# Performance work log

Hardware: AMD Instinct MI355X
Metric: run time of the kernel (lower is better)

Reference implementation:

```python
import jax, jax.numpy as jnp
import numpy as np

N, D, HF, HS, E, TOPK = 4096, 1024, 2048, 4096, 8, 2
NUM_FRACTAL = 4  # int(8 * 0.5)
EPS_RMS = 1e-6


def setup_inputs() -> dict:
    key = jax.random.key(0)
    ks = jax.random.split(key, 9)
    s = 0.02
    return {
        "x": jax.random.normal(ks[0], (N, D), dtype=jnp.float32),
        "router_w": jax.random.normal(ks[1], (E, D), dtype=jnp.float32) * s,
        "frac_rms": jnp.ones((NUM_FRACTAL, D), jnp.float32),
        "frac_w1": jax.random.normal(ks[2], (NUM_FRACTAL, HF, D), dtype=jnp.float32) * s,
        "frac_w2": jax.random.normal(ks[3], (NUM_FRACTAL, D, HF), dtype=jnp.float32) * s,
        "frac_w3": jax.random.normal(ks[4], (NUM_FRACTAL, HF, D), dtype=jnp.float32) * s,
        "frac_gamma": jnp.full((NUM_FRACTAL, D), 1e-5, jnp.float32),
        "sw_w1": jax.random.normal(ks[5], (E - NUM_FRACTAL, HS, D), dtype=jnp.float32) * s,
        "sw_w2": jax.random.normal(ks[6], (E - NUM_FRACTAL, D, HS), dtype=jnp.float32) * s,
        "sw_w3": jax.random.normal(ks[7], (E - NUM_FRACTAL, HS, D), dtype=jnp.float32) * s,
    }


def _rmsnorm(x, w):
    return x * jax.lax.rsqrt(jnp.mean(x * x, axis=-1, keepdims=True) + EPS_RMS) * w


def _swiglu(x, w1, w2, w3):
    # torch Linear: y = x @ W.T
    return (jax.nn.silu(x @ w1.T) * (x @ w3.T)) @ w2.T


def _fractal(x, rms_w, w1, w2, w3, gamma):
    # depth=1 FractalBlock, eval mode (stochastic depth = identity)
    xn = _rmsnorm(x, rms_w)
    xn = xn + _swiglu(xn, w1, w2, w3)
    return gamma * xn + x


def _moe(x, router_w, frac_rms, frac_w1, frac_w2, frac_w3, frac_gamma,
         sw_w1, sw_w2, sw_w3):
    gate_logits = x @ router_w.T                      # [N, E]
    weights = jax.nn.softmax(gate_logits, axis=-1)
    top_w, top_i = jax.lax.top_k(weights, TOPK)        # [N, K]
    top_w = top_w / jnp.maximum(jnp.sum(top_w, axis=-1, keepdims=True), 1e-9)
    # dense combine weights: zero for unrouted experts (mathematically equal
    # to the gather/index_add dispatch in the original)
    combine = jnp.zeros((x.shape[0], E), x.dtype).at[
        jnp.arange(x.shape[0])[:, None], top_i].add(top_w)  # [N, E]

    out = jnp.zeros_like(x)
    for e in range(NUM_FRACTAL):
        out = out + combine[:, e:e + 1] * _fractal(
            x, frac_rms[e], frac_w1[e], frac_w2[e], frac_w3[e], frac_gamma[e])
    for j in range(E - NUM_FRACTAL):
        e = NUM_FRACTAL + j
        out = out + combine[:, e:e + 1] * _swiglu(x, sw_w1[j], sw_w2[j], sw_w3[j])
    return out


def reference(x, router_w, frac_rms, frac_w1, frac_w2, frac_w3, frac_gamma,
              sw_w1, sw_w2, sw_w3):
    return _moe(x, router_w, frac_rms, frac_w1, frac_w2, frac_w3, frac_gamma,
                sw_w1, sw_w2, sw_w3)
```

## Files before the change

### kernel.cpp

```cpp
#include <hip/hip_runtime.h>
#include <stdint.h>

#define N_TOK 4096
#define DIM   1024
#define HFRAC 2048
#define HSW   4096
#define NEXP  8
#define NFRAC 4
#define TOPK  2
#define TOTAL_ROWS (N_TOK * TOPK)
#define PAD_ROWS   (TOTAL_ROWS + 128)

typedef unsigned short u16;
typedef __bf16 bf16x8 __attribute__((ext_vector_type(8)));
typedef float  floatx4 __attribute__((ext_vector_type(4)));

struct alignas(8)  us4 { u16 v[4]; };

__device__ __forceinline__ u16 f32_to_bf16_raw(float f) {
    union { float f; uint32_t u; } v; v.f = f;
    uint32_t u = v.u;
    uint32_t r = 0x7FFFu + ((u >> 16) & 1u);
    return (u16)((u + r) >> 16);
}
__device__ __forceinline__ float bf16_raw_to_f32(u16 h) {
    union { uint32_t u; float f; } v; v.u = ((uint32_t)h) << 16;
    return v.f;
}

__device__ __forceinline__ void gload16(const void* g, void* l) {
    __builtin_amdgcn_global_load_lds(
        (const __attribute__((address_space(1))) void*)g,
        (__attribute__((address_space(3))) void*)l, 16, 0, 0);
}

__device__ __forceinline__ int sw_addr(int row, int chunk) {
    return row * 64 + ((chunk ^ (row & 7)) << 3);
}

__global__ __launch_bounds__(256) void router_kernel(
    const float* __restrict__ x, const float* __restrict__ rw,
    int* __restrict__ re, float* __restrict__ rc, int* __restrict__ counts) {
    const int token = blockIdx.x * 4 + (threadIdx.x >> 6);
    const int lane  = threadIdx.x & 63;
    const float* xr = x + (size_t)token * DIM;

    float acc[NEXP];
#pragma unroll
    for (int e = 0; e < NEXP; ++e) acc[e] = 0.0f;
#pragma unroll
    for (int i = 0; i < DIM / 64; ++i) {
        int k = lane + i * 64;
        float xv = xr[k];
#pragma unroll
        for (int e = 0; e < NEXP; ++e) acc[e] += xv * rw[e * DIM + k];
    }
#pragma unroll
    for (int e = 0; e < NEXP; ++e) {
#pragma unroll
        for (int off = 32; off > 0; off >>= 1) acc[e] += __shfl_down(acc[e], off);
    }
    if (lane == 0) {
        float mx = acc[0];
#pragma unroll
        for (int e = 1; e < NEXP; ++e) mx = fmaxf(mx, acc[e]);
        float w[NEXP]; float s = 0.0f;
#pragma unroll
        for (int e = 0; e < NEXP; ++e) { w[e] = expf(acc[e] - mx); s += w[e]; }
        float inv = 1.0f / s;
#pragma unroll
        for (int e = 0; e < NEXP; ++e) w[e] *= inv;
        int i1 = 0;
#pragma unroll
        for (int e = 1; e < NEXP; ++e) if (w[e] > w[i1]) i1 = e;
        int i2 = (i1 == 0) ? 1 : 0;
#pragma unroll
        for (int e = 0; e < NEXP; ++e) if (e != i1 && w[e] > w[i2]) i2 = e;
        float denom = fmaxf(w[i1] + w[i2], 1e-9f);
        re[token]         = i1; rc[token]         = w[i1] / denom;
        re[N_TOK + token] = i2; rc[N_TOK + token] = w[i2] / denom;
        atomicAdd(&counts[i1], 1);
        atomicAdd(&counts[i2], 1);
    }
}

__global__ void offsets_kernel(const int* __restrict__ counts,
                               int* __restrict__ offs) {
    if (threadIdx.x == 0 && blockIdx.x == 0) {
        int a = 0;
#pragma unroll
        for (int e = 0; e < NEXP; ++e) { offs[e] = a; a += counts[e]; }
    }
}

__global__ __launch_bounds__(256) void scatter_kernel(
    const int* __restrict__ re, const float* __restrict__ rc,
    const int* __restrict__ offs, int* __restrict__ cursor,
    int* __restrict__ rowtok, float* __restrict__ co) {
    int token = blockIdx.x * 256 + threadIdx.x;
#pragma unroll
    for (int slot = 0; slot < TOPK; ++slot) {
        int e = re[slot * N_TOK + token];
        int i = atomicAdd(&cursor[e], 1);
        int r = offs[e] + i;
        rowtok[r] = token | (slot << 16);
        co[r]     = rc[slot * N_TOK + token];
    }
}

__global__ __launch_bounds__(256) void gather_norm_kernel(
    const float* __restrict__ x, const float* __restrict__ frac_rms,
    const int* __restrict__ rowtok, const int* __restrict__ offs,
    u16* __restrict__ Ag) {
    const int r   = blockIdx.x;
    const int tid = threadIdx.x;
    if (r >= TOTAL_ROWS) {
        us4 z = {0, 0, 0, 0};
        reinterpret_cast<us4*>(Ag + (size_t)r * DIM)[tid] = z;
        return;
    }
    int e = 0;
#pragma unroll
    for (int i = 1; i < NEXP; ++i) if (r >= offs[i]) e = i;
    const int token = rowtok[r] & 0xFFFF;
    float4 v = reinterpret_cast<const float4*>(x + (size_t)token * DIM)[tid];
    if (e < NFRAC) {
        float ss = v.x * v.x + v.y * v.y + v.z * v.z + v.w * v.w;
#pragma unroll
        for (int off = 32; off > 0; off >>= 1) ss += __shfl_down(ss, off);
        __shared__ float red[4];
        if ((tid & 63) == 0) red[tid >> 6] = ss;
        __syncthreads();
        float scale = rsqrtf((red[0] + red[1] + red[2] + red[3]) * (1.0f / DIM) + 1e-6f);
        float4 wv = reinterpret_cast<const float4*>(frac_rms + (size_t)e * DIM)[tid];
        v.x *= scale * wv.x; v.y *= scale * wv.y;
        v.z *= scale * wv.z; v.w *= scale * wv.w;
    }
    us4 o = { f32_to_bf16_raw(v.x), f32_to_bf16_raw(v.y),
              f32_to_bf16_raw(v.z), f32_to_bf16_raw(v.w) };
    reinterpret_cast<us4*>(Ag + (size_t)r * DIM)[tid] = o;
}

#define FA4 (NFRAC * HFRAC * DIM / 4)
#define SA4 ((NEXP - NFRAC) * HSW * DIM / 4)
#define CVT_BLOCKS ((FA4 + SA4) / 256)

__global__ __launch_bounds__(256) void cvt_pair_kernel(
    const float* __restrict__ a, const float* __restrict__ b,
    u16* __restrict__ dst) {
    size_t i = (size_t)blockIdx.x * 256 + threadIdx.x;
    const float4* src; size_t off;
    if (i < (size_t)FA4) { src = (const float4*)a; off = i; }
    else                 { src = (const float4*)b; off = i - FA4; }
    float4 v = src[off];
    us4 o = { f32_to_bf16_raw(v.x), f32_to_bf16_raw(v.y),
              f32_to_bf16_raw(v.z), f32_to_bf16_raw(v.w) };
    reinterpret_cast<us4*>(dst)[i] = o;
}

#define BM 128
#define BN 64
#define BK 64

__global__ __launch_bounds__(256, 4) void gemm1_kernel(
    const u16* __restrict__ Ag, const u16* __restrict__ W1b,
    const u16* __restrict__ W3b, u16* __restrict__ gbuf,
    const int* __restrict__ counts, const int* __restrict__ offs) {
    const int e   = blockIdx.y;
    const int cnt = counts[e];
    const int m0  = blockIdx.z * BM;
    if (m0 >= cnt) return;
    const int Ne = (e < NFRAC) ? HFRAC : HSW;
    const int n0 = blockIdx.x * BN;
    if (n0 >= Ne) return;
    const int rowbase = offs[e];
    const size_t wofs = (e < NFRAC)
        ? (size_t)e * HFRAC * DIM
        : (size_t)NFRAC * HFRAC * DIM + (size_t)(e - NFRAC) * HSW * DIM;
    const u16* W1 = W1b + wofs + (size_t)n0 * DIM;
    const u16* W3 = W3b + wofs + (size_t)n0 * DIM;
    const u16* A  = Ag + (size_t)(rowbase + m0) * DIM;

    __shared__ u16 sA[BM * BK];
    __shared__ u16 sB1[BN * BK];
    __shared__ u16 sB3[BN * BK];

    const int tid  = threadIdx.x;
    const int lane = tid & 63;
    const int wave = tid >> 6;
    const int wr   = wave >> 1, wc = wave & 1;
    const int rlo  = lane & 15, khi = lane >> 4;

    floatx4 acc1[4][2], acc3[4][2];
    floatx4 zero = { 0.f, 0.f, 0.f, 0.f };
#pragma unroll
    for (int mt = 0; mt < 4; ++mt)
#pragma unroll
        for (int nt = 0; nt < 2; ++nt) { acc1[mt][nt] = zero; acc3[mt][nt] = zero; }

    for (int k0 = 0; k0 < DIM; k0 += BK) {
#pragma unroll
        for (int it = 0; it < 4; ++it) {
            int ci = it * 256 + tid;
            int r = ci >> 3, cc = ci & 7;
            int csw = ((cc ^ (r & 7)) << 3);
            gload16(A + (size_t)r * DIM + k0 + csw, &sA[ci * 8]);
        }
#pragma unroll
        for (int it = 0; it < 2; ++it) {
            int ci = it * 256 + tid;
            int r = ci >> 3, cc = ci & 7;
            int csw = ((cc ^ (r & 7)) << 3);
            gload16(W1 + (size_t)r * DIM + k0 + csw, &sB1[ci * 8]);
            gload16(W3 + (size_t)r * DIM + k0 + csw, &sB3[ci * 8]);
        }
        __syncthreads();
#pragma unroll
        for (int ks = 0; ks < 2; ++ks) {
            const int kk = ks * 4 + khi;
            bf16x8 af[4], b1[2], b3[2];
#pragma unroll
            for (int t = 0; t < 4; ++t)
                af[t] = *reinterpret_cast<const bf16x8*>(&sA[sw_addr(wr * 64 + t * 16 + rlo, kk)]);
#pragma unroll
            for (int t = 0; t < 2; ++t) {
                b1[t] = *reinterpret_cast<const bf16x8*>(&sB1[sw_addr(wc * 32 + t * 16 + rlo, kk)]);
                b3[t] = *reinterpret_cast<const bf16x8*>(&sB3[sw_addr(wc * 32 + t * 16 + rlo, kk)]);
            }
#pragma unroll
            for (int mt = 0; mt < 4; ++mt)
#pragma unroll
                for (int nt = 0; nt < 2; ++nt) {
                    acc1[mt][nt] = __builtin_amdgcn_mfma_f32_16x16x32_bf16(
                        af[mt], b1[nt], acc1[mt][nt], 0, 0, 0);
                    acc3[mt][nt] = __builtin_amdgcn_mfma_f32_16x16x32_bf16(
                        af[mt], b3[nt], acc3[mt][nt], 0, 0, 0);
                }
        }
        __syncthreads();
    }
#pragma unroll
    for (int mt = 0; mt < 4; ++mt)
#pragma unroll
        for (int nt = 0; nt < 2; ++nt)
#pragma unroll
            for (int r = 0; r < 4; ++r) {
                int row_local = m0 + wr * 64 + mt * 16 + khi * 4 + r;
                if (row_local >= cnt) continue;
                int col = n0 + wc * 32 + nt * 16 + rlo;
                float h1 = acc1[mt][nt][r];
                float h3 = acc3[mt][nt][r];
                float g = (h1 / (1.0f + expf(-h1))) * h3;
                gbuf[(size_t)(rowbase + row_local) * HSW + col] = f32_to_bf16_raw(g);
            }
}

__global__ __launch_bounds__(256, 6) void gemm2_kernel(
    const u16* __restrict__ gbuf, const u16* __restrict__ W2b,
    const u16* __restrict__ Ag, const float* __restrict__ x,
    const float* __restrict__ frac_gamma,
    const int* __restrict__ rowtok, const float* __restrict__ co,
    const int* __restrict__ counts, const int* __restrict__ offs,
    float* __restrict__ out) {
    const int e   = blockIdx.y;
    const int cnt = counts[e];
    const int m0  = blockIdx.z * BM;
    if (m0 >= cnt) return;
    const int n0 = blockIdx.x * BN;
    const int Ke = (e < NFRAC) ? HFRAC : HSW;
    const int rowbase = offs[e];
    const size_t wofs = (e < NFRAC)
        ? (size_t)e * DIM * HFRAC
        : (size_t)NFRAC * DIM * HFRAC + (size_t)(e - NFRAC) * DIM * HSW;
    const u16* W2 = W2b + wofs + (size_t)n0 * Ke;
    const u16* A  = gbuf + (size_t)(rowbase + m0) * HSW;

    __shared__ u16 sA[BM * BK];
    __shared__ u16 sB[BN * BK];

    const int tid  = threadIdx.x;
    const int lane = tid & 63;
    const int wave = tid >> 6;
    const int wr   = wave >> 1, wc = wave & 1;
    const int rlo  = lane & 15, khi = lane >> 4;

    floatx4 acc[4][2];
    floatx4 zero = { 0.f, 0.f, 0.f, 0.f };
#pragma unroll
    for (int mt = 0; mt < 4; ++mt)
#pragma unroll
        for (int nt = 0; nt < 2; ++nt) acc[mt][nt] = zero;

    for (int k0 = 0; k0 < Ke; k0 += BK) {
#pragma unroll
        for (int it = 0; it < 4; ++it) {
            int ci = it * 256 + tid;
            int r = ci >> 3, cc = ci & 7;
            int csw = ((cc ^ (r & 7)) << 3);
            gload16(A + (size_t)r * HSW + k0 + csw, &sA[ci * 8]);
        }
#pragma unroll
        for (int it = 0; it < 2; ++it) {
            int ci = it * 256 + tid;
            int r = ci >> 3, cc = ci & 7;
            int csw = ((cc ^ (r & 7)) << 3);
            gload16(W2 + (size_t)r * Ke + k0 + csw, &sB[ci * 8]);
        }
        __syncthreads();
#pragma unroll
        for (int ks = 0; ks < 2; ++ks) {
            const int kk = ks * 4 + khi;
            bf16x8 af[4], bf[2];
#pragma unroll
            for (int t = 0; t < 4; ++t)
                af[t] = *reinterpret_cast<const bf16x8*>(&sA[sw_addr(wr * 64 + t * 16 + rlo, kk)]);
#pragma unroll
            for (int t = 0; t < 2; ++t)
                bf[t] = *reinterpret_cast<const bf16x8*>(&sB[sw_addr(wc * 32 + t * 16 + rlo, kk)]);
#pragma unroll
            for (int mt = 0; mt < 4; ++mt)
#pragma unroll
                for (int nt = 0; nt < 2; ++nt)
                    acc[mt][nt] = __builtin_amdgcn_mfma_f32_16x16x32_bf16(
                        af[mt], bf[nt], acc[mt][nt], 0, 0, 0);
        }
        __syncthreads();
    }
    const float* gamma = frac_gamma + (size_t)e * DIM;
#pragma unroll
    for (int mt = 0; mt < 4; ++mt)
#pragma unroll
        for (int nt = 0; nt < 2; ++nt)
#pragma unroll
            for (int rr = 0; rr < 4; ++rr) {
                int row_local = m0 + wr * 64 + mt * 16 + khi * 4 + rr;
                if (row_local >= cnt) continue;
                int r = rowbase + row_local;
                int col = n0 + wc * 32 + nt * 16 + rlo;
                int token = rowtok[r] & 0xFFFF;
                float coef = co[r];
                float y = acc[mt][nt][rr];
                float val;
                if (e < NFRAC) {
                    float xn = bf16_raw_to_f32(Ag[(size_t)r * DIM + col]);
                    val = coef * (gamma[col] * (xn + y) + x[(size_t)token * DIM + col]);
                } else {
                    val = coef * y;
                }
                atomicAdd(&out[(size_t)token * DIM + col], val);
            }
}

extern "C" void kernel_launch(void* const* d_in, const int* in_sizes, int n_in,
                              void* d_out, int out_size, void* d_ws, size_t ws_size,
                              hipStream_t stream) {
    const float* x          = (const float*)d_in[0];
    const float* router_w   = (const float*)d_in[1];
    const float* frac_rms   = (const float*)d_in[2];
    const float* frac_w1    = (const float*)d_in[3];
    const float* frac_w2    = (const float*)d_in[4];
    const float* frac_w3    = (const float*)d_in[5];
    const float* frac_gamma = (const float*)d_in[6];
    const float* sw_w1      = (const float*)d_in[7];
    const float* sw_w2      = (const float*)d_in[8];
    const float* sw_w3      = (const float*)d_in[9];
    float* out = (float*)d_out;

    char* ws = (char*)d_ws;
    int*   counts = (int*)ws;
    int*   cursor = (int*)(ws + 32);
    int*   offs   = (int*)(ws + 64);
    int*   re     = (int*)(ws + 256);
    float* rc     = (float*)(ws + 256 + (32u << 10));
    int*   rowtok = (int*)(ws + 256 + (64u << 10));
    float* co     = (float*)(ws + 256 + (112u << 10));
    u16*   Ag     = (u16*)(ws + (1u << 18));
    u16*   gbuf   = (u16*)(ws + (size_t)18  * (1u << 20));
    u16*   W1b    = (u16*)(ws + (size_t)84  * (1u << 20));
    u16*   W3b    = (u16*)(ws + (size_t)132 * (1u << 20));
    u16*   W2b    = (u16*)(ws + (size_t)84  * (1u << 20));

    hipMemsetAsync(ws, 0, 256, stream);
    hipMemsetAsync(out, 0, (size_t)N_TOK * DIM * 4, stream);

    cvt_pair_kernel<<<CVT_BLOCKS, 256, 0, stream>>>(frac_w1, sw_w1, W1b);
    cvt_pair_kernel<<<CVT_BLOCKS, 256, 0, stream>>>(frac_w3, sw_w3, W3b);

    router_kernel<<<N_TOK / 4, 256, 0, stream>>>(x, router_w, re, rc, counts);
    offsets_kernel<<<1, 64, 0, stream>>>(counts, offs);
    scatter_kernel<<<N_TOK / 256, 256, 0, stream>>>(re, rc, offs, cursor, rowtok, co);
    gather_norm_kernel<<<PAD_ROWS, 256, 0, stream>>>(x, frac_rms, rowtok, offs, Ag);

    gemm1_kernel<<<dim3(HSW / BN, NEXP, TOTAL_ROWS / BM), 256, 0, stream>>>(
        Ag, W1b, W3b, gbuf, counts, offs);

    cvt_pair_kernel<<<CVT_BLOCKS, 256, 0, stream>>>(frac_w2, sw_w2, W2b);

    gemm2_kernel<<<dim3(DIM / BN, NEXP, TOTAL_ROWS / BM), 256, 0, stream>>>(
        gbuf, W2b, Ag, x, frac_gamma, rowtok, co, counts, offs, out);
}
```

Measured before the change: 744.0 us.

## Widen gemm2 N tile, split-K for swiglu experts, merge W1/W3 conversions

The down-projection GEMM now uses 128-wide N tiles, so each wave computes a 64x64 sub-tile with 4x4 MFMA accumulators. For the SwiGLU experts, whose K is 4096, the K range is split in two across blockIdx.z, and the partial sums are combined by the existing atomicAdd into the output. Fractal-expert blocks with odd z exit early. The two fp32-to-bf16 weight conversions for W1 and W3 are merged into a single launch; in exchange gemm2 uses more registers and its launch bound drops to 3 blocks per SIMD.

```diff
diff --git a/kernel.cpp b/kernel.cpp
--- a/kernel.cpp
+++ b/kernel.cpp
@@ -143,7 +143,8 @@
 
 #define FA4 (NFRAC * HFRAC * DIM / 4)
 #define SA4 ((NEXP - NFRAC) * HSW * DIM / 4)
-#define CVT_BLOCKS ((FA4 + SA4) / 256)
+#define CVT_TOT (FA4 + SA4)
+#define CVT_BLOCKS (CVT_TOT / 256)
 
 __global__ __launch_bounds__(256) void cvt_pair_kernel(
     const float* __restrict__ a, const float* __restrict__ b,
@@ -158,8 +159,26 @@
     reinterpret_cast<us4*>(dst)[i] = o;
 }
 
+__global__ __launch_bounds__(256) void cvt_two_kernel(
+    const float* __restrict__ fa, const float* __restrict__ sa,
+    u16* __restrict__ da,
+    const float* __restrict__ fb, const float* __restrict__ sb,
+    u16* __restrict__ db) {
+    size_t i = (size_t)blockIdx.x * 256 + threadIdx.x;
+    const float* f = fa; const float* s = sa; u16* d = da;
+    if (i >= (size_t)CVT_TOT) { i -= CVT_TOT; f = fb; s = sb; d = db; }
+    const float4* src; size_t off;
+    if (i < (size_t)FA4) { src = (const float4*)f; off = i; }
+    else                 { src = (const float4*)s; off = i - FA4; }
+    float4 v = src[off];
+    us4 o = { f32_to_bf16_raw(v.x), f32_to_bf16_raw(v.y),
+              f32_to_bf16_raw(v.z), f32_to_bf16_raw(v.w) };
+    reinterpret_cast<us4*>(d)[i] = o;
+}
+
 #define BM 128
 #define BN 64
+#define BN2 128
 #define BK 64
 
 __global__ __launch_bounds__(256, 4) void gemm1_kernel(
@@ -255,7 +274,7 @@
             }
 }
 
-__global__ __launch_bounds__(256, 6) void gemm2_kernel(
+__global__ __launch_bounds__(256, 3) void gemm2_kernel(
     const u16* __restrict__ gbuf, const u16* __restrict__ W2b,
     const u16* __restrict__ Ag, const float* __restrict__ x,
     const float* __restrict__ frac_gamma,
@@ -264,10 +283,15 @@
     float* __restrict__ out) {
     const int e   = blockIdx.y;
     const int cnt = counts[e];
-    const int m0  = blockIdx.z * BM;
+    const int z   = blockIdx.z;
+    const int m0  = (z >> 1) * BM;
+    const int kp  = z & 1;
     if (m0 >= cnt) return;
-    const int n0 = blockIdx.x * BN;
     const int Ke = (e < NFRAC) ? HFRAC : HSW;
+    int kbeg, kend;
+    if (e < NFRAC) { if (kp) return; kbeg = 0; kend = Ke; }
+    else           { kbeg = kp * (Ke / 2); kend = kbeg + Ke / 2; }
+    const int n0 = blockIdx.x * BN2;
     const int rowbase = offs[e];
     const size_t wofs = (e < NFRAC)
         ? (size_t)e * DIM * HFRAC
@@ -276,7 +300,7 @@
     const u16* A  = gbuf + (size_t)(rowbase + m0) * HSW;
 
     __shared__ u16 sA[BM * BK];
-    __shared__ u16 sB[BN * BK];
+    __shared__ u16 sB[BN2 * BK];
 
     const int tid  = threadIdx.x;
     const int lane = tid & 63;
@@ -284,59 +308,53 @@
     const int wr   = wave >> 1, wc = wave & 1;
     const int rlo  = lane & 15, khi = lane >> 4;
 
-    floatx4 acc[4][2];
+    floatx4 acc[4][4];
     floatx4 zero = { 0.f, 0.f, 0.f, 0.f };
 #pragma unroll
     for (int mt = 0; mt < 4; ++mt)
 #pragma unroll
-        for (int nt = 0; nt < 2; ++nt) acc[mt][nt] = zero;
-
-    for (int k0 = 0; k0 < Ke; k0 += BK) {
+        for (int nt = 0; nt < 4; ++nt) acc[mt][nt] = zero;
+
+    for (int k0 = kbeg; k0 < kend; k0 += BK) {
 #pragma unroll
         for (int it = 0; it < 4; ++it) {
             int ci = it * 256 + tid;
             int r = ci >> 3, cc = ci & 7;
             int csw = ((cc ^ (r & 7)) << 3);
-            gload16(A + (size_t)r * HSW + k0 + csw, &sA[ci * 8]);
-        }
-#pragma unroll
-        for (int it = 0; it < 2; ++it) {
-            int ci = it * 256 + tid;
-            int r = ci >> 3, cc = ci & 7;
-            int csw = ((cc ^ (r & 7)) << 3);
-            gload16(W2 + (size_t)r * Ke + k0 + csw, &sB[ci * 8]);
+            gload16(A  + (size_t)r * HSW + k0 + csw, &sA[ci * 8]);
+            gload16(W2 + (size_t)r * Ke  + k0 + csw, &sB[ci * 8]);
         }
         __syncthreads();
 #pragma unroll
         for (int ks = 0; ks < 2; ++ks) {
             const int kk = ks * 4 + khi;
-            bf16x8 af[4], bf[2];
-#pragma unroll
-            for (int t = 0; t < 4; ++t)
+            bf16x8 af[4], bf[4];
+#pragma unroll
+            for (int t = 0; t < 4; ++t) {
                 af[t] = *reinterpret_cast<const bf16x8*>(&sA[sw_addr(wr * 64 + t * 16 + rlo, kk)]);
-#pragma unroll
-            for (int t = 0; t < 2; ++t)
-                bf[t] = *reinterpret_cast<const bf16x8*>(&sB[sw_addr(wc * 32 + t * 16 + rlo, kk)]);
+                bf[t] = *reinterpret_cast<const bf16x8*>(&sB[sw_addr(wc * 64 + t * 16 + rlo, kk)]);
+            }
 #pragma unroll
             for (int mt = 0; mt < 4; ++mt)
 #pragma unroll
-                for (int nt = 0; nt < 2; ++nt)
+                for (int nt = 0; nt < 4; ++nt)
                     acc[mt][nt] = __builtin_amdgcn_mfma_f32_16x16x32_bf16(
                         af[mt], bf[nt], acc[mt][nt], 0, 0, 0);
         }
         __syncthreads();
     }
     const float* gamma = frac_gamma + (size_t)e * DIM;
+    const bool base = (kbeg == 0);
 #pragma unroll
     for (int mt = 0; mt < 4; ++mt)
 #pragma unroll
-        for (int nt = 0; nt < 2; ++nt)
+        for (int nt = 0; nt < 4; ++nt)
 #pragma unroll
             for (int rr = 0; rr < 4; ++rr) {
                 int row_local = m0 + wr * 64 + mt * 16 + khi * 4 + rr;
                 if (row_local >= cnt) continue;
                 int r = rowbase + row_local;
-                int col = n0 + wc * 32 + nt * 16 + rlo;
+                int col = n0 + wc * 64 + nt * 16 + rlo;
                 int token = rowtok[r] & 0xFFFF;
                 float coef = co[r];
                 float y = acc[mt][nt][rr];
@@ -346,6 +364,7 @@
                     val = coef * (gamma[col] * (xn + y) + x[(size_t)token * DIM + col]);
                 } else {
                     val = coef * y;
+                    (void)base;
                 }
                 atomicAdd(&out[(size_t)token * DIM + col], val);
             }
@@ -383,8 +402,8 @@
     hipMemsetAsync(ws, 0, 256, stream);
     hipMemsetAsync(out, 0, (size_t)N_TOK * DIM * 4, stream);
 
-    cvt_pair_kernel<<<CVT_BLOCKS, 256, 0, stream>>>(frac_w1, sw_w1, W1b);
-    cvt_pair_kernel<<<CVT_BLOCKS, 256, 0, stream>>>(frac_w3, sw_w3, W3b);
+    cvt_two_kernel<<<2 * CVT_BLOCKS, 256, 0, stream>>>(
+        frac_w1, sw_w1, W1b, frac_w3, sw_w3, W3b);
 
     router_kernel<<<N_TOK / 4, 256, 0, stream>>>(x, router_w, re, rc, counts);
     offsets_kernel<<<1, 64, 0, stream>>>(counts, offs);
@@ -396,6 +415,6 @@
 
     cvt_pair_kernel<<<CVT_BLOCKS, 256, 0, stream>>>(frac_w2, sw_w2, W2b);
 
-    gemm2_kernel<<<dim3(DIM / BN, NEXP, TOTAL_ROWS / BM), 256, 0, stream>>>(
+    gemm2_kernel<<<dim3(DIM / BN2, NEXP, (TOTAL_ROWS / BM) * 2), 256, 0, stream>>>(
         gbuf, W2b, Ag, x, frac_gamma, rowtok, co, counts, offs, out);
 }
```

New measurement: 747.2 us. About the same (+0.4%).

## Triple-buffer gemm2 LDS tiles with async prefetch and merge W1/W3 conversions

Applied to the files above, without the earlier changes.

The second GEMM's K loop now uses three LDS buffers and prefetches two tiles ahead. Partial vmcnt waits and a single barrier per iteration replace the previous load/sync/compute/sync pattern, so global loads overlap with MFMA work. The launch-bounds occupancy hint drops from 6 to 2 to allow for the larger LDS footprint. The two W1/W3 fp32-to-bf16 conversion launches are also fused into one kernel, saving a launch.

```diff
diff --git a/kernel.cpp b/kernel.cpp
--- a/kernel.cpp
+++ b/kernel.cpp
@@ -143,7 +143,8 @@
 
 #define FA4 (NFRAC * HFRAC * DIM / 4)
 #define SA4 ((NEXP - NFRAC) * HSW * DIM / 4)
-#define CVT_BLOCKS ((FA4 + SA4) / 256)
+#define CVT_TOT (FA4 + SA4)
+#define CVT_BLOCKS (CVT_TOT / 256)
 
 __global__ __launch_bounds__(256) void cvt_pair_kernel(
     const float* __restrict__ a, const float* __restrict__ b,
@@ -156,6 +157,23 @@
     us4 o = { f32_to_bf16_raw(v.x), f32_to_bf16_raw(v.y),
               f32_to_bf16_raw(v.z), f32_to_bf16_raw(v.w) };
     reinterpret_cast<us4*>(dst)[i] = o;
+}
+
+__global__ __launch_bounds__(256) void cvt_two_kernel(
+    const float* __restrict__ fa, const float* __restrict__ sa,
+    u16* __restrict__ da,
+    const float* __restrict__ fb, const float* __restrict__ sb,
+    u16* __restrict__ db) {
+    size_t i = (size_t)blockIdx.x * 256 + threadIdx.x;
+    const float* f = fa; const float* s = sa; u16* d = da;
+    if (i >= (size_t)CVT_TOT) { i -= CVT_TOT; f = fb; s = sb; d = db; }
+    const float4* src; size_t off;
+    if (i < (size_t)FA4) { src = (const float4*)f; off = i; }
+    else                 { src = (const float4*)s; off = i - FA4; }
+    float4 v = src[off];
+    us4 o = { f32_to_bf16_raw(v.x), f32_to_bf16_raw(v.y),
+              f32_to_bf16_raw(v.z), f32_to_bf16_raw(v.w) };
+    reinterpret_cast<us4*>(d)[i] = o;
 }
 
 #define BM 128
@@ -255,7 +273,7 @@
             }
 }
 
-__global__ __launch_bounds__(256, 6) void gemm2_kernel(
+__global__ __launch_bounds__(256, 2) void gemm2_kernel(
     const u16* __restrict__ gbuf, const u16* __restrict__ W2b,
     const u16* __restrict__ Ag, const float* __restrict__ x,
     const float* __restrict__ frac_gamma,
@@ -275,8 +293,8 @@
     const u16* W2 = W2b + wofs + (size_t)n0 * Ke;
     const u16* A  = gbuf + (size_t)(rowbase + m0) * HSW;
 
-    __shared__ u16 sA[BM * BK];
-    __shared__ u16 sB[BN * BK];
+    __shared__ u16 sA[3][BM * BK];
+    __shared__ u16 sB[3][BN * BK];
 
     const int tid  = threadIdx.x;
     const int lane = tid & 63;
@@ -291,32 +309,45 @@
 #pragma unroll
         for (int nt = 0; nt < 2; ++nt) acc[mt][nt] = zero;
 
-    for (int k0 = 0; k0 < Ke; k0 += BK) {
+    const int NT = Ke / BK;
+
+    auto stage = [&](int b, int kt) {
+        const int k0 = kt * BK;
 #pragma unroll
         for (int it = 0; it < 4; ++it) {
             int ci = it * 256 + tid;
             int r = ci >> 3, cc = ci & 7;
             int csw = ((cc ^ (r & 7)) << 3);
-            gload16(A + (size_t)r * HSW + k0 + csw, &sA[ci * 8]);
+            gload16(A + (size_t)r * HSW + k0 + csw, &sA[b][ci * 8]);
         }
 #pragma unroll
         for (int it = 0; it < 2; ++it) {
             int ci = it * 256 + tid;
             int r = ci >> 3, cc = ci & 7;
             int csw = ((cc ^ (r & 7)) << 3);
-            gload16(W2 + (size_t)r * Ke + k0 + csw, &sB[ci * 8]);
-        }
-        __syncthreads();
+            gload16(W2 + (size_t)r * Ke + k0 + csw, &sB[b][ci * 8]);
+        }
+    };
+
+    stage(0, 0);
+    stage(1, 1);
+    asm volatile("s_waitcnt vmcnt(6)" ::: "memory");
+    __builtin_amdgcn_s_barrier();
+
+    int b = 0;
+    for (int t = 0; t < NT; ++t) {
+        const int bn = (b == 0) ? 2 : b - 1;
+        if (t + 2 < NT) stage(bn, t + 2);
 #pragma unroll
         for (int ks = 0; ks < 2; ++ks) {
             const int kk = ks * 4 + khi;
             bf16x8 af[4], bf[2];
 #pragma unroll
-            for (int t = 0; t < 4; ++t)
-                af[t] = *reinterpret_cast<const bf16x8*>(&sA[sw_addr(wr * 64 + t * 16 + rlo, kk)]);
-#pragma unroll
-            for (int t = 0; t < 2; ++t)
-                bf[t] = *reinterpret_cast<const bf16x8*>(&sB[sw_addr(wc * 32 + t * 16 + rlo, kk)]);
+            for (int tt = 0; tt < 4; ++tt)
+                af[tt] = *reinterpret_cast<const bf16x8*>(&sA[b][sw_addr(wr * 64 + tt * 16 + rlo, kk)]);
+#pragma unroll
+            for (int tt = 0; tt < 2; ++tt)
+                bf[tt] = *reinterpret_cast<const bf16x8*>(&sB[b][sw_addr(wc * 32 + tt * 16 + rlo, kk)]);
 #pragma unroll
             for (int mt = 0; mt < 4; ++mt)
 #pragma unroll
@@ -324,8 +355,16 @@
                     acc[mt][nt] = __builtin_amdgcn_mfma_f32_16x16x32_bf16(
                         af[mt], bf[nt], acc[mt][nt], 0, 0, 0);
         }
-        __syncthreads();
-    }
+        if (t + 2 < NT) {
+            asm volatile("s_waitcnt vmcnt(6)" ::: "memory");
+            __builtin_amdgcn_s_barrier();
+        } else if (t + 1 < NT) {
+            asm volatile("s_waitcnt vmcnt(0)" ::: "memory");
+            __builtin_amdgcn_s_barrier();
+        }
+        b = (b == 2) ? 0 : b + 1;
+    }
+
     const float* gamma = frac_gamma + (size_t)e * DIM;
 #pragma unroll
     for (int mt = 0; mt < 4; ++mt)
@@ -383,8 +422,8 @@
     hipMemsetAsync(ws, 0, 256, stream);
     hipMemsetAsync(out, 0, (size_t)N_TOK * DIM * 4, stream);
 
-    cvt_pair_kernel<<<CVT_BLOCKS, 256, 0, stream>>>(frac_w1, sw_w1, W1b);
-    cvt_pair_kernel<<<CVT_BLOCKS, 256, 0, stream>>>(frac_w3, sw_w3, W3b);
+    cvt_two_kernel<<<2 * CVT_BLOCKS, 256, 0, stream>>>(
+        frac_w1, sw_w1, W1b, frac_w3, sw_w3, W3b);
 
     router_kernel<<<N_TOK / 4, 256, 0, stream>>>(x, router_w, re, rc, counts);
     offsets_kernel<<<1, 64, 0, stream>>>(counts, offs);
```

Measured after the change: 804.4 us. 8.1% more time.
